# Optimization experiments

Hardware: AMD Instinct MI355X
Metric: run time of the kernel (lower is better)

Reference implementation:

```python
import jax, jax.numpy as jnp
import numpy as np

TOP_X = 3
M = 10
K = 10
BETA = 2.0
EPS = 1e-12  # matches torch F.normalize eps


def setup_inputs() -> dict:
    key = jax.random.key(0)
    kq, kd = jax.random.split(key)
    query_features = jax.random.normal(kq, (128, 512), dtype=jnp.float32)
    db = jax.random.normal(kd, (100000, 512), dtype=jnp.float32)
    return {"query_features": query_features, "db": db}


def _get_top_k(q, db, k):
    # Dense inner-product kNN: q [n, D], db [N, D] -> ([n, k, D], [n, k], [n, k])
    s = q @ db.T                      # [n, N]
    ts, ti = jax.lax.top_k(s, k)      # [n, k]
    return db[ti], ts, ti


def reference(query_features, db):
    B, D = query_features.shape
    # First-level retrieval: top-M neighbors of each query
    top_m, _, top_m_ids = _get_top_k(query_features, db, M)       # [B, M, D]
    # Query expansion: elementwise max over query + its top K-1 neighbors
    top_k = top_m[:, : K - 1]                                     # [B, K-1, D]
    query_top_k = jnp.max(
        jnp.concatenate((query_features[:, None, :], top_k), axis=1), axis=1
    )                                                              # [B, D]
    # Second-level retrieval: top-K neighbors of each of the B*M candidates
    top_k_m, top_k_m_scores, _ = _get_top_k(top_m.reshape(-1, D), db, K)
    top_k_m = top_k_m.reshape(B, M, K, D)
    top_k_m_scores = top_k_m_scores.reshape(B, M, K)
    # Prepend the query itself (weight 1) to each neighbor set
    exp_q = jnp.broadcast_to(query_features[:, None, None, :], (B, M, 1, D))
    top_k_m = jnp.concatenate((exp_q, top_k_m), axis=2)            # [B, M, K+1, D]
    ones = jnp.ones((B, M, 1), dtype=query_features.dtype)
    scores_all = jnp.concatenate((ones, top_k_m_scores), axis=2)   # [B, M, K+1]
    # Weighted neighbor aggregation (SuperGlobal refinement)
    weights = scores_all * BETA
    weighted_sum = jnp.einsum('bmkd,bmk->bmd', top_k_m, weights)   # [B, M, D]
    norm_factor = 1.0 + jnp.sum(weights, axis=2, keepdims=True)    # [B, M, 1]
    top_m_refined = weighted_sum / norm_factor
    # L2 normalize refined candidates and expanded query
    top_m_refined = top_m_refined / jnp.clip(
        jnp.linalg.norm(top_m_refined, axis=-1, keepdims=True), EPS)
    query_top_k = query_top_k / jnp.clip(
        jnp.linalg.norm(query_top_k, axis=-1, keepdims=True), EPS)
    # Rerank scores
    score_1 = jnp.einsum('bmd,bd->bm', top_m_refined, query_features)
    score_2 = jnp.einsum('bmd,bd->bm', top_m_refined, query_top_k)
    final_scores = (score_1 + score_2) * 0.5                        # [B, M]
    top_x_scores, top_x_indices = jax.lax.top_k(final_scores, TOP_X)
    top_x_ids = jnp.take_along_axis(top_m_ids, top_x_indices, axis=1)
    return (top_x_ids, top_x_scores)
```

## Files before the change

### kernel.cpp

```cpp
#include <hip/hip_runtime.h>
#include <math.h>

#define NQ    128
#define ND    512
#define NDB   100000
#define NDBP  100096
#define MM    10
#define KK    10
#define TOPX  3
#define R2    (NQ * MM)

#define QB1    128
#define NB1    64
#define NCH1   (NDBP / NB1)
#define QB2    256
#define NB     128
#define KT     64
#define NKIT   (ND / KT)
#define NCHUNK (NDBP / NB)
#define CVTBLKS ((int)(((size_t)NDBP * ND / 16 + 255) / 256))

#define Z0    3.125f
#define Z2    3.3f
#define QSC   32.0f
#define CAP   384
#define NROWT (NQ + R2)

typedef int i32x4 __attribute__((ext_vector_type(4)));

#define PIPE_BAR(VM) asm volatile("s_waitcnt vmcnt(" #VM ")\n\ts_barrier" ::: "memory")
#define LGKM_BAR()   asm volatile("s_waitcnt lgkmcnt(0)\n\ts_barrier" ::: "memory")

__device__ __forceinline__ void gload_lds16(const void* gsrc, void* ldst) {
    __builtin_amdgcn_global_load_lds(
        (const __attribute__((address_space(1))) unsigned int*)gsrc,
        (__attribute__((address_space(3))) unsigned int*)ldst, 16, 0, 0);
}

__device__ __forceinline__ signed char f2i8(float x) {
    int v = (int)rintf(x * QSC);
    v = v > 127 ? 127 : v;
    v = v < -127 ? -127 : v;
    return (signed char)v;
}

__global__ __launch_bounds__(256) void cvt_prep_kernel(
    const float* __restrict__ db, signed char* __restrict__ out,
    const float* __restrict__ q, signed char* __restrict__ qi8,
    int* __restrict__ thrI, int* __restrict__ cnt)
{
    if ((int)blockIdx.x < CVTBLKS) {
        const size_t i = ((size_t)blockIdx.x * 256 + threadIdx.x) * 16;
        if (i >= (size_t)NDBP * ND) return;
        union { signed char c[16]; i32x4 v; } u;
        if (i + 16 <= (size_t)NDB * ND) {
#pragma unroll
            for (int j = 0; j < 4; ++j) {
                const float4 f = *(const float4*)(db + i + j * 4);
                u.c[j * 4 + 0] = f2i8(f.x);
                u.c[j * 4 + 1] = f2i8(f.y);
                u.c[j * 4 + 2] = f2i8(f.z);
                u.c[j * 4 + 3] = f2i8(f.w);
            }
        } else {
#pragma unroll
            for (int j = 0; j < 16; ++j) u.c[j] = 0;
        }
        *(i32x4*)(out + i) = u.v;
    } else {
        const int row = (int)blockIdx.x - CVTBLKS;
        const int t = (int)threadIdx.x;
        __shared__ float red[4];
        const float a = q[(size_t)row * ND + t];
        const float b = q[(size_t)row * ND + t + 256];
        qi8[(size_t)row * ND + t] = f2i8(a);
        qi8[(size_t)row * ND + t + 256] = f2i8(b);
        float ss = a * a + b * b;
        for (int off = 32; off; off >>= 1) ss += __shfl_xor(ss, off);
        if ((t & 63) == 0) red[t >> 6] = ss;
        __syncthreads();
        if (t == 0) {
            const float tot = red[0] + red[1] + red[2] + red[3];
            thrI[row] = (int)(QSC * QSC * Z0 * sqrtf(tot));
            cnt[row] = 0;
        }
    }
}

__global__ __launch_bounds__(256) void prep_q_kernel(
    const float* __restrict__ src, signed char* __restrict__ dst,
    int* __restrict__ thrI, int* __restrict__ cnt)
{
    const int row = blockIdx.x;
    const int t = (int)threadIdx.x;
    __shared__ float red[4];
    const float a = src[(size_t)row * ND + t];
    const float b = src[(size_t)row * ND + t + 256];
    dst[(size_t)row * ND + t] = f2i8(a);
    dst[(size_t)row * ND + t + 256] = f2i8(b);
    float ss = a * a + b * b;
    for (int off = 32; off; off >>= 1) ss += __shfl_xor(ss, off);
    if ((t & 63) == 0) red[t >> 6] = ss;
    __syncthreads();
    if (t == 0) {
        const float tot = red[0] + red[1] + red[2] + red[3];
        thrI[row] = (int)(QSC * QSC * Z0 * sqrtf(tot));
        cnt[row] = 0;
    }
}

__global__ __launch_bounds__(256) void gemm1_kernel(
    const signed char* __restrict__ Qb,
    const signed char* __restrict__ Db,
    const int* __restrict__ thrI,
    int* __restrict__ candCnt, int* __restrict__ candId)
{
    __shared__ char lds[24576];
    __shared__ int thrS[QB1];

    const int tid = (int)threadIdx.x;
    const int ln = tid & 63;
    const int wv = tid >> 6;
    const int wr = wv >> 1;
    const int wc = wv & 1;
    const int n0 = blockIdx.x * NB1;

    if (tid < QB1) thrS[tid] = thrI[tid];

    i32x4 acc[4][2] = {};

    auto stageQ = [&](int kc, int buf) {
#pragma unroll
        for (int c = 0; c < 2; ++c) {
            const int U = c * 256 + tid;
            const int r = U >> 2;
            const int u = (U & 3) ^ ((r >> 1) & 3);
            gload_lds16(Qb + (size_t)r * ND + kc + u * 16,
                        lds + buf * 12288 + U * 16);
        }
    };
    auto stageD = [&](int kc, int buf) {
        const int U = tid;
        const int r = U >> 2;
        const int u = (U & 3) ^ ((r >> 1) & 3);
        gload_lds16(Db + (size_t)(n0 + r) * ND + kc + u * 16,
                    lds + buf * 12288 + 8192 + U * 16);
    };
    auto compute = [&](int buf) {
        const char* Qt = lds + buf * 12288;
        const char* Dt = Qt + 8192;
        i32x4 a[4], b[2];
#pragma unroll
        for (int qt = 0; qt < 4; ++qt) {
            const int r = wr * 64 + qt * 16 + (ln & 15);
            const int u = (ln >> 4) ^ ((r >> 1) & 3);
            a[qt] = *(const i32x4*)(Qt + r * 64 + u * 16);
        }
#pragma unroll
        for (int nt = 0; nt < 2; ++nt) {
            const int r = wc * 32 + nt * 16 + (ln & 15);
            const int u = (ln >> 4) ^ ((r >> 1) & 3);
            b[nt] = *(const i32x4*)(Dt + r * 64 + u * 16);
        }
        __builtin_amdgcn_s_setprio(1);
#pragma unroll
        for (int qt = 0; qt < 4; ++qt)
#pragma unroll
            for (int nt = 0; nt < 2; ++nt)
                acc[qt][nt] = __builtin_amdgcn_mfma_i32_16x16x64_i8(
                    a[qt], b[nt], acc[qt][nt], 0, 0, 0);
        __builtin_amdgcn_s_setprio(0);
    };

    __syncthreads();
    stageQ(0, 0); stageD(0, 0);
    stageQ(KT, 1); stageD(KT, 1);
#pragma unroll
    for (int it = 0; it < NKIT; ++it) {
        if (it < NKIT - 1) PIPE_BAR(3); else PIPE_BAR(0);
        const int buf = it & 1;
        compute(buf);
        LGKM_BAR();
        if (it + 2 < NKIT) { stageQ((it + 2) * KT, buf); stageD((it + 2) * KT, buf); }
    }

    const int lg = ln >> 4;
    const int lc = ln & 15;
#pragma unroll
    for (int qt = 0; qt < 4; ++qt) {
#pragma unroll
        for (int c = 0; c < 4; ++c) {
            const int rloc = wr * 64 + qt * 16 + lg * 4 + c;
            const int T = thrS[rloc];
#pragma unroll
            for (int nt = 0; nt < 2; ++nt) {
                const int v = acc[qt][nt][c];
                if (v > T) {
                    const int n = n0 + wc * 32 + nt * 16 + lc;
                    if (n < NDB) {
                        const int slot = atomicAdd(&candCnt[rloc], 1);
                        if (slot < CAP) candId[(size_t)rloc * CAP + slot] = n;
                    }
                }
            }
        }
    }
}

__global__ __launch_bounds__(512) void gemm2s_kernel(
    const signed char* __restrict__ Qb,
    const signed char* __restrict__ Db,
    const int* __restrict__ thrI,
    int* __restrict__ candCnt, int* __restrict__ candId)
{
    const int bid = (int)blockIdx.x;
    const int xcd = bid & 7;
    const int slot = bid >> 3;
    const int nch_x = (xcd < 6) ? 98 : 97;
    if (slot >= nch_x * 5) return;
    const int cstart = (xcd < 6) ? 98 * xcd : 98 * 6 + 97 * (xcd - 6);
    const int chunk = cstart + slot / 5;
    const int qtile = slot % 5;

    __shared__ char lds[49152];
    __shared__ int thrS[QB2];

    const int tid = (int)threadIdx.x;
    const int ln = tid & 63;
    const int wv = tid >> 6;
    const int wr = wv >> 1;
    const int wc = wv & 1;
    const int q0 = qtile * QB2;
    const int n0 = chunk * NB;

    if (tid < QB2) thrS[tid] = thrI[q0 + tid];

    i32x4 acc[4][4] = {};

    auto stageQ = [&](int kc, int buf) {
#pragma unroll
        for (int c = 0; c < 2; ++c) {
            const int U = c * 512 + tid;
            const int r = U >> 2;
            const int u = (U & 3) ^ ((r >> 1) & 3);
            gload_lds16(Qb + (size_t)(q0 + r) * ND + kc + u * 16,
                        lds + buf * 24576 + U * 16);
        }
    };
    auto stageD = [&](int kc, int buf) {
        const int U = tid;
        const int r = U >> 2;
        const int u = (U & 3) ^ ((r >> 1) & 3);
        gload_lds16(Db + (size_t)(n0 + r) * ND + kc + u * 16,
                    lds + buf * 24576 + 16384 + U * 16);
    };
    auto compute = [&](int buf) {
        const char* Qt = lds + buf * 24576;
        const char* Dt = Qt + 16384;
        i32x4 a[4], b[4];
#pragma unroll
        for (int qt = 0; qt < 4; ++qt) {
            const int r = wr * 64 + qt * 16 + (ln & 15);
            const int u = (ln >> 4) ^ ((r >> 1) & 3);
            a[qt] = *(const i32x4*)(Qt + r * 64 + u * 16);
        }
#pragma unroll
        for (int nt = 0; nt < 4; ++nt) {
            const int r = wc * 64 + nt * 16 + (ln & 15);
            const int u = (ln >> 4) ^ ((r >> 1) & 3);
            b[nt] = *(const i32x4*)(Dt + r * 64 + u * 16);
        }
        __builtin_amdgcn_s_setprio(1);
#pragma unroll
        for (int qt = 0; qt < 4; ++qt)
#pragma unroll
            for (int nt = 0; nt < 4; ++nt)
                acc[qt][nt] = __builtin_amdgcn_mfma_i32_16x16x64_i8(
                    a[qt], b[nt], acc[qt][nt], 0, 0, 0);
        __builtin_amdgcn_s_setprio(0);
    };

    __syncthreads();
    stageQ(0, 0); stageD(0, 0);
    stageQ(KT, 1); stageD(KT, 1);
#pragma unroll
    for (int it = 0; it < NKIT; ++it) {
        if (it < NKIT - 1) PIPE_BAR(3); else PIPE_BAR(0);
        const int buf = it & 1;
        compute(buf);
        LGKM_BAR();
        if (it + 2 < NKIT) { stageQ((it + 2) * KT, buf); stageD((it + 2) * KT, buf); }
    }

    const int lg = ln >> 4;
    const int lc = ln & 15;
#pragma unroll
    for (int qt = 0; qt < 4; ++qt) {
#pragma unroll
        for (int c = 0; c < 4; ++c) {
            const int rloc = wr * 64 + qt * 16 + lg * 4 + c;
            const int row = q0 + rloc;
            const int T = thrS[rloc];
#pragma unroll
            for (int nt = 0; nt < 4; ++nt) {
                const int v = acc[qt][nt][c];
                if (v > T) {
                    const int n = n0 + wc * 64 + nt * 16 + lc;
                    if (n < NDB) {
                        const int slot2 = atomicAdd(&candCnt[row], 1);
                        if (slot2 < CAP) candId[(size_t)row * CAP + slot2] = n;
                    }
                }
            }
        }
    }
}

__global__ __launch_bounds__(512) void gemm2_cvt_kernel(
    const signed char* __restrict__ Qb, const float* __restrict__ Df,
    const int* __restrict__ thrI, int* __restrict__ candCnt, int* __restrict__ candId,
    int qrows)
{
    __shared__ char lds[49152];
    __shared__ int thrS[QB2];
    const int tid = (int)threadIdx.x;
    const int ln = tid & 63;
    const int wv = tid >> 6;
    const int wr = wv >> 1;
    const int wc = wv & 1;
    const int q0 = blockIdx.x * QB2;
    const int n0 = blockIdx.y * NB;
    if (tid < QB2 && q0 + tid < qrows) thrS[tid] = thrI[q0 + tid];
    else if (tid < QB2) thrS[tid] = 0x7fffffff;

    i32x4 acc[4][4] = {};
    auto stageQ = [&](int kc, int buf) {
#pragma unroll
        for (int c = 0; c < 2; ++c) {
            const int U = c * 512 + tid;
            const int r = U >> 2;
            const int u = (U & 3) ^ ((r >> 1) & 3);
            const int gq = q0 + r;
            if (gq < qrows)
                gload_lds16(Qb + (size_t)gq * ND + kc + u * 16,
                            lds + buf * 24576 + U * 16);
            else
                *(i32x4*)(lds + buf * 24576 + U * 16) = i32x4{0, 0, 0, 0};
        }
    };
    auto stageDcvt = [&](int kc, int buf) {
        const int U = tid;
        const int r = U >> 2;
        const int u = (U & 3) ^ ((r >> 1) & 3);
        const int gn = n0 + r;
        union { signed char cc[16]; i32x4 v; } w;
        if (gn < NDB) {
#pragma unroll
            for (int j = 0; j < 4; ++j) {
                const float4 f = *(const float4*)(Df + (size_t)gn * ND + kc + u * 16 + j * 4);
                w.cc[j * 4 + 0] = f2i8(f.x);
                w.cc[j * 4 + 1] = f2i8(f.y);
                w.cc[j * 4 + 2] = f2i8(f.z);
                w.cc[j * 4 + 3] = f2i8(f.w);
            }
        } else {
#pragma unroll
            for (int j = 0; j < 16; ++j) w.cc[j] = 0;
        }
        *(i32x4*)(lds + buf * 24576 + 16384 + U * 16) = w.v;
    };
    stageQ(0, 0); stageDcvt(0, 0);
    for (int it = 0; it < NKIT; ++it) {
        const int buf = it & 1;
        __syncthreads();
        if (it + 1 < NKIT) { stageQ((it + 1) * KT, buf ^ 1); stageDcvt((it + 1) * KT, buf ^ 1); }
        const char* Qt = lds + buf * 24576;
        const char* Dt = Qt + 16384;
        i32x4 a[4], b[4];
#pragma unroll
        for (int qt = 0; qt < 4; ++qt) {
            const int r = wr * 64 + qt * 16 + (ln & 15);
            const int u = (ln >> 4) ^ ((r >> 1) & 3);
            a[qt] = *(const i32x4*)(Qt + r * 64 + u * 16);
        }
#pragma unroll
        for (int nt = 0; nt < 4; ++nt) {
            const int r = wc * 64 + nt * 16 + (ln & 15);
            const int u = (ln >> 4) ^ ((r >> 1) & 3);
            b[nt] = *(const i32x4*)(Dt + r * 64 + u * 16);
        }
#pragma unroll
        for (int qt = 0; qt < 4; ++qt)
#pragma unroll
            for (int nt = 0; nt < 4; ++nt)
                acc[qt][nt] = __builtin_amdgcn_mfma_i32_16x16x64_i8(
                    a[qt], b[nt], acc[qt][nt], 0, 0, 0);
        __syncthreads();
    }
    const int lg = ln >> 4;
    const int lc = ln & 15;
#pragma unroll
    for (int qt = 0; qt < 4; ++qt) {
#pragma unroll
        for (int c = 0; c < 4; ++c) {
            const int rloc = wr * 64 + qt * 16 + lg * 4 + c;
            const int row = q0 + rloc;
            if (row >= qrows) continue;
            const int T = thrS[rloc];
#pragma unroll
            for (int nt = 0; nt < 4; ++nt) {
                const int v = acc[qt][nt][c];
                if (v > T) {
                    const int n = n0 + wc * 64 + nt * 16 + lc;
                    if (n < NDB) {
                        const int slot = atomicAdd(&candCnt[row], 1);
                        if (slot < CAP) candId[(size_t)row * CAP + slot] = n;
                    }
                }
            }
        }
    }
}

__device__ __forceinline__ void rescore_cands(
    const float* __restrict__ db, const int* __restrict__ candId,
    size_t base, int nc, int wv, int ln,
    const float* qs, float* sc, int* sid)
{
    const float4 qa = *(const float4*)&qs[ln * 8];
    const float4 qb = *(const float4*)&qs[ln * 8 + 4];
    for (int i0 = wv * 2; i0 < nc; i0 += 8) {
        const int i1 = i0 + 1;
        const bool has1 = (i1 < nc);
        const int idA = candId[base + i0];
        const int idB = has1 ? candId[base + i1] : idA;
        const float4* dA = (const float4*)(db + (size_t)idA * ND);
        const float4* dB = (const float4*)(db + (size_t)idB * ND);
        const float4 a0 = dA[ln * 2];
        const float4 a1 = dA[ln * 2 + 1];
        const float4 b0 = dB[ln * 2];
        const float4 b1 = dB[ln * 2 + 1];
        float sA = qa.x * a0.x + qa.y * a0.y + qa.z * a0.z + qa.w * a0.w
                 + qb.x * a1.x + qb.y * a1.y + qb.z * a1.z + qb.w * a1.w;
        float sB = qa.x * b0.x + qa.y * b0.y + qa.z * b0.z + qa.w * b0.w
                 + qb.x * b1.x + qb.y * b1.y + qb.z * b1.z + qb.w * b1.w;
        for (int off = 32; off; off >>= 1) {
            sA += __shfl_xor(sA, off);
            sB += __shfl_xor(sB, off);
        }
        if (ln == 0) {
            sc[i0] = sA; sid[i0] = idA;
            if (has1) { sc[i1] = sB; sid[i1] = idB; }
        }
    }
}

__global__ __launch_bounds__(256) void rescore_fuse_kernel(
    const float* __restrict__ Qf,
    const float* __restrict__ db,
    const int* __restrict__ candCnt, const int* __restrict__ candId,
    int* __restrict__ s1I,
    signed char* __restrict__ q2i8,
    float* __restrict__ qtk,
    int* __restrict__ thrI2, int* __restrict__ cnt2)
{
    const int b = blockIdx.x;
    const int tid = (int)threadIdx.x;
    const int ln = tid & 63;
    const int wv = tid >> 6;

    __shared__ float qs[ND];
    __shared__ float sc[CAP];
    __shared__ int   sid[CAP];
    __shared__ float rbs[4];
    __shared__ int   rbi[4], rbsl[4];
    __shared__ int   topI[MM];
    __shared__ float red[11][4];

    qs[tid] = Qf[(size_t)b * ND + tid];
    qs[tid + 256] = Qf[(size_t)b * ND + tid + 256];
    const int nc = min(candCnt[b], CAP);
    for (int i = tid; i < CAP; i += 256) { sc[i] = -INFINITY; sid[i] = 0x7fffffff; }
    __syncthreads();

    rescore_cands(db, candId, (size_t)b * CAP, nc, wv, ln, qs, sc, sid);
    __syncthreads();

    for (int it = 0; it < KK; ++it) {
        float bs = -INFINITY;
        int bid = 0x7fffffff, bsl = -1;
        for (int i = tid; i < nc; i += 256) {
            const float s = sc[i];
            if (s > bs || (s == bs && sid[i] < bid)) { bs = s; bid = sid[i]; bsl = i; }
        }
        for (int off = 32; off; off >>= 1) {
            const float os = __shfl_xor(bs, off);
            const int oi = __shfl_xor(bid, off);
            const int osl = __shfl_xor(bsl, off);
            if (os > bs || (os == bs && oi < bid)) { bs = os; bid = oi; bsl = osl; }
        }
        if (ln == 0) { rbs[wv] = bs; rbi[wv] = bid; rbsl[wv] = bsl; }
        __syncthreads();
        if (tid == 0) {
            float fb = -INFINITY; int fi = 0x7fffffff, fs = -1;
#pragma unroll
            for (int w = 0; w < 4; ++w) {
                if (rbs[w] > fb || (rbs[w] == fb && rbi[w] < fi)) {
                    fb = rbs[w]; fi = rbi[w]; fs = rbsl[w];
                }
            }
            const int idw = (fi == 0x7fffffff) ? 0 : fi;
            s1I[b * MM + it] = idw;
            topI[it] = idw;
            if (fs >= 0) sc[fs] = -INFINITY;
        }
        __syncthreads();
    }

    const float q0v = qs[tid];
    const float q1v = qs[tid + 256];
    float mx0 = q0v, mx1 = q1v;
    float ssq[MM];
#pragma unroll
    for (int m = 0; m < MM; ++m) {
        const int id = topI[m];
        const float v0 = db[(size_t)id * ND + tid];
        const float v1 = db[(size_t)id * ND + tid + 256];
        const size_t rowo = (size_t)(b * MM + m) * ND;
        q2i8[rowo + tid] = f2i8(v0);
        q2i8[rowo + tid + 256] = f2i8(v1);
        ssq[m] = v0 * v0 + v1 * v1;
        if (m < KK - 1) { mx0 = fmaxf(mx0, v0); mx1 = fmaxf(mx1, v1); }
    }
    float sqq = mx0 * mx0 + mx1 * mx1;
#pragma unroll
    for (int m = 0; m < MM; ++m) {
        float s = ssq[m];
        for (int off = 32; off; off >>= 1) s += __shfl_xor(s, off);
        if (ln == 0) red[m][wv] = s;
    }
    for (int off = 32; off; off >>= 1) sqq += __shfl_xor(sqq, off);
    if (ln == 0) red[10][wv] = sqq;
    __syncthreads();
    if (tid < MM) {
        const float tot = red[tid][0] + red[tid][1] + red[tid][2] + red[tid][3];
        thrI2[b * MM + tid] = (int)(QSC * QSC * Z2 * sqrtf(tot));
        cnt2[b * MM + tid] = 0;
    }
    const float tq = red[10][0] + red[10][1] + red[10][2] + red[10][3];
    const float inv = 1.0f / fmaxf(sqrtf(tq), 1e-12f);
    qtk[(size_t)b * ND + tid] = mx0 * inv;
    qtk[(size_t)b * ND + tid + 256] = mx1 * inv;
}

__global__ __launch_bounds__(256) void rescore_refine_kernel(
    const int* __restrict__ s1I,
    const float* __restrict__ q,
    const float* __restrict__ qtk,
    const float* __restrict__ db,
    const int* __restrict__ candCnt, const int* __restrict__ candId,
    float* __restrict__ finalS)
{
    const int row = blockIdx.x;
    const int b = row / MM;
    const int tid = (int)threadIdx.x;
    const int ln = tid & 63;
    const int wv = tid >> 6;

    __shared__ float qs[ND];
    __shared__ float sc[CAP];
    __shared__ int   sid[CAP];
    __shared__ float rbs[4];
    __shared__ int   rbi[4], rbsl[4];
    __shared__ float topS[KK];
    __shared__ int   topI[KK];
    __shared__ float red[3][4];

    const int qid = s1I[row];
    qs[tid] = db[(size_t)qid * ND + tid];
    qs[tid + 256] = db[(size_t)qid * ND + tid + 256];
    const int nc = min(candCnt[row], CAP);
    for (int i = tid; i < CAP; i += 256) { sc[i] = -INFINITY; sid[i] = 0x7fffffff; }
    __syncthreads();

    rescore_cands(db, candId, (size_t)row * CAP, nc, wv, ln, qs, sc, sid);
    __syncthreads();

    for (int it = 0; it < KK; ++it) {
        float bs = -INFINITY;
        int bid = 0x7fffffff, bsl = -1;
        for (int i = tid; i < nc; i += 256) {
            const float s = sc[i];
            if (s > bs || (s == bs && sid[i] < bid)) { bs = s; bid = sid[i]; bsl = i; }
        }
        for (int off = 32; off; off >>= 1) {
            const float os = __shfl_xor(bs, off);
            const int oi = __shfl_xor(bid, off);
            const int osl = __shfl_xor(bsl, off);
            if (os > bs || (os == bs && oi < bid)) { bs = os; bid = oi; bsl = osl; }
        }
        if (ln == 0) { rbs[wv] = bs; rbi[wv] = bid; rbsl[wv] = bsl; }
        __syncthreads();
        if (tid == 0) {
            float fb = -INFINITY; int fi = 0x7fffffff, fs = -1;
#pragma unroll
            for (int w = 0; w < 4; ++w) {
                if (rbs[w] > fb || (rbs[w] == fb && rbi[w] < fi)) {
                    fb = rbs[w]; fi = rbi[w]; fs = rbsl[w];
                }
            }
            if (!(fb > -INFINITY)) { fb = 0.f; fi = 0; }
            topS[it] = fb;
            topI[it] = (fi == 0x7fffffff) ? 0 : fi;
            if (fs >= 0) sc[fs] = -INFINITY;
        }
        __syncthreads();
    }

    float ssum = 0.f;
#pragma unroll
    for (int m = 0; m < KK; ++m) ssum += topS[m];
    const float nf = 3.f + 2.f * ssum;

    const float q0v = q[(size_t)b * ND + tid];
    const float q1v = q[(size_t)b * ND + tid + 256];
    float w0 = 2.f * q0v;
    float w1 = 2.f * q1v;
#pragma unroll
    for (int m = 0; m < KK; ++m) {
        const int id = topI[m];
        const float w = 2.f * topS[m];
        w0 = fmaf(w, db[(size_t)id * ND + tid], w0);
        w1 = fmaf(w, db[(size_t)id * ND + tid + 256], w1);
    }
    w0 /= nf;
    w1 /= nf;

    float s_n = w0 * w0 + w1 * w1;
    float s_1 = w0 * q0v + w1 * q1v;
    float s_2 = w0 * qtk[(size_t)b * ND + tid] + w1 * qtk[(size_t)b * ND + tid + 256];
    for (int off = 32; off; off >>= 1) {
        s_n += __shfl_xor(s_n, off);
        s_1 += __shfl_xor(s_1, off);
        s_2 += __shfl_xor(s_2, off);
    }
    if (ln == 0) { red[0][wv] = s_n; red[1][wv] = s_1; red[2][wv] = s_2; }
    __syncthreads();
    if (tid == 0) {
        const float tn = red[0][0] + red[0][1] + red[0][2] + red[0][3];
        const float t1 = red[1][0] + red[1][1] + red[1][2] + red[1][3];
        const float t2 = red[2][0] + red[2][1] + red[2][2] + red[2][3];
        const float inv = 1.0f / fmaxf(sqrtf(tn), 1e-12f);
        finalS[row] = 0.5f * (t1 * inv + t2 * inv);
    }
}

__global__ __launch_bounds__(64) void final_topk_kernel(
    const float* __restrict__ finalS, const int* __restrict__ s1I,
    float* __restrict__ out)
{
    const int b = blockIdx.x * 64 + (int)threadIdx.x;
    if (b >= NQ) return;
    float s[MM];
#pragma unroll
    for (int m = 0; m < MM; ++m) s[m] = finalS[b * MM + m];
#pragma unroll
    for (int x = 0; x < TOPX; ++x) {
        float bs = -INFINITY;
        int bm = 0;
#pragma unroll
        for (int m = 0; m < MM; ++m) {
            if (s[m] > bs) { bs = s[m]; bm = m; }
        }
        out[b * TOPX + x] = (float)s1I[b * MM + bm];
        out[NQ * TOPX + b * TOPX + x] = bs;
        s[bm] = -INFINITY;
    }
}

extern "C" void kernel_launch(void* const* d_in, const int* in_sizes, int n_in,
                              void* d_out, int out_size, void* d_ws, size_t ws_size,
                              hipStream_t stream)
{
    const float* q = (const float*)d_in[0];
    const float* db = (const float*)d_in[1];
    float* out = (float*)d_out;

    char* ws = (char*)d_ws;
    size_t off = 0;
    auto alloc = [&](size_t bytes) -> void* {
        void* p = ws + off;
        off += (bytes + 255) & ~(size_t)255;
        return p;
    };
    signed char* qi8  = (signed char*)alloc((size_t)NQ * ND);
    signed char* q2i8 = (signed char*)alloc((size_t)R2 * ND);
    float* qtk  = (float*)alloc(sizeof(float) * NQ * ND);
    int*   thrI = (int*)alloc(sizeof(int) * NROWT);
    int*   cnt  = (int*)alloc(sizeof(int) * NROWT);
    int*   cid  = (int*)alloc(sizeof(int) * (size_t)NROWT * CAP);
    int*   s1I  = (int*)alloc(sizeof(int) * NQ * MM);
    float* fS   = (float*)alloc(sizeof(float) * NQ * MM);
    signed char* dbi8 = (signed char*)alloc((size_t)NDBP * ND);
    const bool pathA = (ws_size >= off);

    if (pathA) {
        cvt_prep_kernel<<<CVTBLKS + NQ, 256, 0, stream>>>(
            db, dbi8, q, qi8, thrI, cnt);
        gemm1_kernel<<<NCH1, 256, 0, stream>>>(qi8, dbi8, thrI, cnt, cid);
    } else {
        prep_q_kernel<<<NQ, 256, 0, stream>>>(q, qi8, thrI, cnt);
        gemm2_cvt_kernel<<<dim3(1, NCHUNK), 512, 0, stream>>>(
            qi8, db, thrI, cnt, cid, NQ);
    }

    rescore_fuse_kernel<<<NQ, 256, 0, stream>>>(
        q, db, cnt, cid, s1I, q2i8, qtk, thrI + NQ, cnt + NQ);

    if (pathA)
        gemm2s_kernel<<<3920, 512, 0, stream>>>(
            q2i8, dbi8, thrI + NQ, cnt + NQ, cid + (size_t)NQ * CAP);
    else
        gemm2_cvt_kernel<<<dim3(R2 / QB2, NCHUNK), 512, 0, stream>>>(
            q2i8, db, thrI + NQ, cnt + NQ, cid + (size_t)NQ * CAP, R2);

    rescore_refine_kernel<<<R2, 256, 0, stream>>>(
        s1I, q, qtk, db, cnt + NQ, cid + (size_t)NQ * CAP, fS);

    final_topk_kernel<<<(NQ + 63) / 64, 64, 0, stream>>>(fS, s1I, out);
    (void)in_sizes; (void)n_in; (void)out_size;
}
```

Measured before the change: 225.7 us.

## Fuse db int8 conversion into stage-1 GEMM kernel with on-the-fly quantized staging

Replaces the separate conversion+prep kernel and the first int8 GEMM with one mega kernel. GEMM blocks read the float db directly and quantize it into LDS, while extra blocks write the int8 db copy for the second stage. The query prep moves to its own small kernel. The intent is to drop the dependency between the conversion and the GEMM and overlap them. In exchange, the GEMM loses its async global-to-LDS pipeline for synchronous loads with barriers and reads four times as many bytes, and db is read twice overall.

```diff
diff --git a/kernel.cpp b/kernel.cpp
--- a/kernel.cpp
+++ b/kernel.cpp
@@ -42,49 +42,6 @@
     v = v > 127 ? 127 : v;
     v = v < -127 ? -127 : v;
     return (signed char)v;
-}
-
-__global__ __launch_bounds__(256) void cvt_prep_kernel(
-    const float* __restrict__ db, signed char* __restrict__ out,
-    const float* __restrict__ q, signed char* __restrict__ qi8,
-    int* __restrict__ thrI, int* __restrict__ cnt)
-{
-    if ((int)blockIdx.x < CVTBLKS) {
-        const size_t i = ((size_t)blockIdx.x * 256 + threadIdx.x) * 16;
-        if (i >= (size_t)NDBP * ND) return;
-        union { signed char c[16]; i32x4 v; } u;
-        if (i + 16 <= (size_t)NDB * ND) {
-#pragma unroll
-            for (int j = 0; j < 4; ++j) {
-                const float4 f = *(const float4*)(db + i + j * 4);
-                u.c[j * 4 + 0] = f2i8(f.x);
-                u.c[j * 4 + 1] = f2i8(f.y);
-                u.c[j * 4 + 2] = f2i8(f.z);
-                u.c[j * 4 + 3] = f2i8(f.w);
-            }
-        } else {
-#pragma unroll
-            for (int j = 0; j < 16; ++j) u.c[j] = 0;
-        }
-        *(i32x4*)(out + i) = u.v;
-    } else {
-        const int row = (int)blockIdx.x - CVTBLKS;
-        const int t = (int)threadIdx.x;
-        __shared__ float red[4];
-        const float a = q[(size_t)row * ND + t];
-        const float b = q[(size_t)row * ND + t + 256];
-        qi8[(size_t)row * ND + t] = f2i8(a);
-        qi8[(size_t)row * ND + t + 256] = f2i8(b);
-        float ss = a * a + b * b;
-        for (int off = 32; off; off >>= 1) ss += __shfl_xor(ss, off);
-        if ((t & 63) == 0) red[t >> 6] = ss;
-        __syncthreads();
-        if (t == 0) {
-            const float tot = red[0] + red[1] + red[2] + red[3];
-            thrI[row] = (int)(QSC * QSC * Z0 * sqrtf(tot));
-            cnt[row] = 0;
-        }
-    }
 }
 
 __global__ __launch_bounds__(256) void prep_q_kernel(
@@ -109,21 +66,45 @@
     }
 }
 
-__global__ __launch_bounds__(256) void gemm1_kernel(
+__global__ __launch_bounds__(256) void stage1_mega_kernel(
     const signed char* __restrict__ Qb,
-    const signed char* __restrict__ Db,
+    const float* __restrict__ Df,
+    signed char* __restrict__ DbOut,
     const int* __restrict__ thrI,
     int* __restrict__ candCnt, int* __restrict__ candId)
 {
     __shared__ char lds[24576];
     __shared__ int thrS[QB1];
 
+    const int bid = (int)blockIdx.x;
     const int tid = (int)threadIdx.x;
+
+    if (bid >= NCH1) {
+        const size_t i = ((size_t)(bid - NCH1) * 256 + tid) * 16;
+        if (i >= (size_t)NDBP * ND) return;
+        union { signed char c[16]; i32x4 v; } u;
+        if (i + 16 <= (size_t)NDB * ND) {
+#pragma unroll
+            for (int j = 0; j < 4; ++j) {
+                const float4 f = *(const float4*)(Df + i + j * 4);
+                u.c[j * 4 + 0] = f2i8(f.x);
+                u.c[j * 4 + 1] = f2i8(f.y);
+                u.c[j * 4 + 2] = f2i8(f.z);
+                u.c[j * 4 + 3] = f2i8(f.w);
+            }
+        } else {
+#pragma unroll
+            for (int j = 0; j < 16; ++j) u.c[j] = 0;
+        }
+        *(i32x4*)(DbOut + i) = u.v;
+        return;
+    }
+
     const int ln = tid & 63;
     const int wv = tid >> 6;
     const int wr = wv >> 1;
     const int wc = wv & 1;
-    const int n0 = blockIdx.x * NB1;
+    const int n0 = bid * NB1;
 
     if (tid < QB1) thrS[tid] = thrI[tid];
 
@@ -139,12 +120,26 @@
                         lds + buf * 12288 + U * 16);
         }
     };
-    auto stageD = [&](int kc, int buf) {
+    auto stageDcvt = [&](int kc, int buf) {
         const int U = tid;
         const int r = U >> 2;
         const int u = (U & 3) ^ ((r >> 1) & 3);
-        gload_lds16(Db + (size_t)(n0 + r) * ND + kc + u * 16,
-                    lds + buf * 12288 + 8192 + U * 16);
+        const int gn = n0 + r;
+        union { signed char cc[16]; i32x4 v; } w;
+        if (gn < NDB) {
+#pragma unroll
+            for (int j = 0; j < 4; ++j) {
+                const float4 f = *(const float4*)(Df + (size_t)gn * ND + kc + u * 16 + j * 4);
+                w.cc[j * 4 + 0] = f2i8(f.x);
+                w.cc[j * 4 + 1] = f2i8(f.y);
+                w.cc[j * 4 + 2] = f2i8(f.z);
+                w.cc[j * 4 + 3] = f2i8(f.w);
+            }
+        } else {
+#pragma unroll
+            for (int j = 0; j < 16; ++j) w.cc[j] = 0;
+        }
+        *(i32x4*)(lds + buf * 12288 + 8192 + U * 16) = w.v;
     };
     auto compute = [&](int buf) {
         const char* Qt = lds + buf * 12288;
@@ -172,16 +167,13 @@
         __builtin_amdgcn_s_setprio(0);
     };
 
-    __syncthreads();
-    stageQ(0, 0); stageD(0, 0);
-    stageQ(KT, 1); stageD(KT, 1);
-#pragma unroll
+    stageQ(0, 0); stageDcvt(0, 0);
     for (int it = 0; it < NKIT; ++it) {
-        if (it < NKIT - 1) PIPE_BAR(3); else PIPE_BAR(0);
         const int buf = it & 1;
+        __syncthreads();
+        if (it + 1 < NKIT) { stageQ((it + 1) * KT, buf ^ 1); stageDcvt((it + 1) * KT, buf ^ 1); }
         compute(buf);
-        LGKM_BAR();
-        if (it + 2 < NKIT) { stageQ((it + 2) * KT, buf); stageD((it + 2) * KT, buf); }
+        __syncthreads();
     }
 
     const int lg = ln >> 4;
@@ -704,12 +696,12 @@
     signed char* dbi8 = (signed char*)alloc((size_t)NDBP * ND);
     const bool pathA = (ws_size >= off);
 
+    prep_q_kernel<<<NQ, 256, 0, stream>>>(q, qi8, thrI, cnt);
+
     if (pathA) {
-        cvt_prep_kernel<<<CVTBLKS + NQ, 256, 0, stream>>>(
-            db, dbi8, q, qi8, thrI, cnt);
-        gemm1_kernel<<<NCH1, 256, 0, stream>>>(qi8, dbi8, thrI, cnt, cid);
+        stage1_mega_kernel<<<NCH1 + CVTBLKS, 256, 0, stream>>>(
+            qi8, db, dbi8, thrI, cnt, cid);
     } else {
-        prep_q_kernel<<<NQ, 256, 0, stream>>>(q, qi8, thrI, cnt);
         gemm2_cvt_kernel<<<dim3(1, NCHUNK), 512, 0, stream>>>(
             qi8, db, thrI, cnt, cid, NQ);
     }
```

After: 228.5 us. About the same (+1.2%).
